# Performance work log

Hardware: AMD Instinct MI355X
Metric: run time of the kernel (lower is better)

The kernel has to match this reference:

```python
import jax, jax.numpy as jnp
import numpy as np

N, G, E, H, OUT, MAX_N = 131072, 256, 384, 6, 256, 1024
DH = E // H  # 64


def _make_sizes():
    # variable-length segments summing exactly to N, each in [1, MAX_N]
    rng = np.random.default_rng(0)
    raw = rng.integers(128, 896, G).astype(np.int64)
    diff = int(N - raw.sum())
    q, r = divmod(diff, G)
    sizes = raw + q
    sizes[:r] += 1
    assert sizes.sum() == N and sizes.min() >= 1 and sizes.max() <= MAX_N
    return sizes


def setup_inputs() -> dict:
    key = jax.random.key(0)
    ks = jax.random.split(key, 8)
    s = 1.0 / np.sqrt(E)
    return {
        "node_feat": jax.random.normal(ks[0], (N, E), jnp.float32),
        "sizes": jnp.asarray(_make_sizes(), jnp.int32),
        "query": jax.random.normal(ks[1], (E,), jnp.float32),
        "Wq": jax.random.normal(ks[2], (E, E), jnp.float32) * s,
        "bq": jnp.zeros((E,), jnp.float32),
        "Wk": jax.random.normal(ks[3], (E, E), jnp.float32) * s,
        "bk": jnp.zeros((E,), jnp.float32),
        "Wv": jax.random.normal(ks[4], (E, E), jnp.float32) * s,
        "bv": jnp.zeros((E,), jnp.float32),
        "Wo": jax.random.normal(ks[5], (E, E), jnp.float32) * s,
        "bo": jnp.zeros((E,), jnp.float32),
        "Wp": jax.random.normal(ks[6], (OUT, E), jnp.float32) * s,
        "bp": jnp.zeros((OUT,), jnp.float32),
    }


def reference(node_feat, sizes, query, Wq, bq, Wk, bk, Wv, bv, Wo, bo, Wp, bp):
    # segment offsets and padded gather indices
    offsets = jnp.cumsum(sizes) - sizes                      # [G]
    pos = jnp.arange(MAX_N)
    idx = jnp.clip(offsets[:, None] + pos[None, :], 0, N - 1)  # [G, MAX_N]
    mask = pos[None, :] < sizes[:, None]                     # [G, MAX_N]

    # project K/V on the flat node table (one big GEMM), then gather into padded form
    k_flat = node_feat @ Wk.T + bk                           # [N, E]
    v_flat = node_feat @ Wv.T + bv
    k = k_flat[idx].reshape(G, MAX_N, H, DH)
    v = v_flat[idx].reshape(G, MAX_N, H, DH)

    # single shared query token, pre-scaled (PyTorch MHA scales q by 1/sqrt(head_dim))
    q = ((query @ Wq.T + bq) * (1.0 / np.sqrt(DH))).reshape(H, DH)

    scores = jnp.einsum('hd,gnhd->ghn', q, k)                # [G, H, MAX_N]
    scores = jnp.where(mask[:, None, :], scores, -1e30)
    attn = jax.nn.softmax(scores, axis=-1)
    pooled = jnp.einsum('ghn,gnhd->ghd', attn, v).reshape(G, E)

    out = pooled @ Wo.T + bo                                 # MHA out_proj
    return out @ Wp.T + bp                                   # final proj  [G, OUT]
```

## Files before the change

### kernel.cpp

```cpp
#include <hip/hip_runtime.h>
#include <math.h>

#define NN 131072
#define G  256
#define E  384
#define H  6
#define DH 64
#define OUTD 256
#define MAXN 1024

#define SPLIT 4
#define PART_STRIDE 2316

#define WS_QK   0
#define WS_OFF  2432
#define WS_PART 12288
#define WS_WVT  (WS_PART + G*SPLIT*PART_STRIDE)
#define WS_WOT  (WS_WVT + E*E)
#define WS_WPT  (WS_WOT + E*E)

__global__ __launch_bounds__(256) void k_prep(
    const int* __restrict__ sizes, const float* __restrict__ query,
    const float* __restrict__ Wq, const float* __restrict__ bq,
    const float* __restrict__ Wk, const float* __restrict__ Wv,
    const float* __restrict__ Wo, const float* __restrict__ Wp,
    float* __restrict__ wsf) {
  const int b = blockIdx.x;
  const int tid = threadIdx.x;
  if (b == 0) {
    __shared__ int s_scan[G];
    const int sz = sizes[tid];
    s_scan[tid] = sz;
    __syncthreads();
    for (int d = 1; d < G; d <<= 1) {
      int t = (tid >= d) ? s_scan[tid - d] : 0;
      __syncthreads();
      s_scan[tid] += t;
      __syncthreads();
    }
    ((int*)(wsf + WS_OFF))[tid] = s_scan[tid] - sz;
  } else if (b <= 36) {
    const int h = (b - 1) / 6, ec = (b - 1) % 6;
    __shared__ float qv_s[64];
    __shared__ float qps[256];
    __shared__ float ps[256];
    {
      const int r = tid >> 2, q = tid & 3;
      const int row = h * 64 + r;
      float a = 0.f;
#pragma unroll 4
      for (int j = 0; j < 96; j++)
        a += Wq[(size_t)row * E + q * 96 + j] * query[q * 96 + j];
      qps[tid] = a;
    }
    __syncthreads();
    if (tid < 64)
      qv_s[tid] = 0.125f * (qps[tid * 4] + qps[tid * 4 + 1] +
                            qps[tid * 4 + 2] + qps[tid * 4 + 3] +
                            bq[h * 64 + tid]);
    __syncthreads();
    const int el = tid & 63, dq = tid >> 6;
    float a = 0.f;
#pragma unroll 4
    for (int d = dq * 16; d < dq * 16 + 16; d++)
      a += qv_s[d] * Wk[(size_t)(h * 64 + d) * E + ec * 64 + el];
    ps[tid] = a;
    __syncthreads();
    if (tid < 64)
      wsf[WS_QK + h * E + ec * 64 + tid] =
          ps[tid] + ps[64 + tid] + ps[128 + tid] + ps[192 + tid];
  } else {
    __shared__ float s[64][65];
    const int t = b - 37;
    const float* src;
    float* dst;
    int R, tr, tc;
    if (t < 36)      { src = Wv; dst = wsf + WS_WVT; R = 384; tr = t / 6;        tc = t % 6; }
    else if (t < 72) { src = Wo; dst = wsf + WS_WOT; R = 384; tr = (t - 36) / 6; tc = (t - 36) % 6; }
    else             { src = Wp; dst = wsf + WS_WPT; R = 256; tr = (t - 72) / 6; tc = (t - 72) % 6; }
    const int r0 = tr * 64, c0 = tc * 64;
#pragma unroll
    for (int k = 0; k < 16; k++) {
      int idx = k * 256 + tid;
      int r = idx >> 6, cc = idx & 63;
      s[r][cc] = src[(size_t)(r0 + r) * E + c0 + cc];
    }
    __syncthreads();
#pragma unroll
    for (int k = 0; k < 16; k++) {
      int idx = k * 256 + tid;
      int cc = idx >> 6, r = idx & 63;
      dst[(size_t)(c0 + cc) * R + r0 + r] = s[r][cc];
    }
  }
}

template <int CTRL>
__device__ __forceinline__ float dpp_radd(float v) {
  int t = __builtin_amdgcn_update_dpp(0, __float_as_int(v), CTRL, 0xf, 0xf, true);
  return v + __int_as_float(t);
}
__device__ __forceinline__ float wave_sum64(float v) {
  v = dpp_radd<0xB1>(v);
  v = dpp_radd<0x4E>(v);
  v = dpp_radd<0x141>(v);
  v = dpp_radd<0x140>(v);
  v += __shfl_xor(v, 16, 64);
  v += __shfl_xor(v, 32, 64);
  return v;
}

__global__ __launch_bounds__(768, 3) void k12s_quarter(
    const float* __restrict__ x, const int* __restrict__ sizes,
    float* __restrict__ wsf) {
  __shared__ float xsl[4][H * E];
  __shared__ float msh[12][H], lsh[12][H], wgts[12][H];
  __shared__ float Msh[H], Lsh[H];

  const int tid = threadIdx.x;
  const int lane = tid & 63;
  const int w = tid >> 6;
  const int b = blockIdx.x;
  const int g = b >> 2, q = b & 3;
  const int sz = sizes[g];
  const int qlen = (sz + 3) >> 2;
  const int start = q * qlen;
  int len = sz - start;
  if (len > qlen) len = qlen;
  if (len < 0) len = 0;
  const int n0 = ((const int*)(wsf + WS_OFF))[g] + start;

  float qk[6][6];
#pragma unroll
  for (int h = 0; h < 6; h++)
#pragma unroll
    for (int k = 0; k < 6; k++) qk[h][k] = wsf[WS_QK + h * E + k * 64 + lane];

  float m[6], l[6], acc[6][6];
#pragma unroll
  for (int h = 0; h < 6; h++) {
    m[h] = -3.0e38f;
    l[h] = 0.f;
#pragma unroll
    for (int k = 0; k < 6; k++) acc[h][k] = 0.f;
  }

  const float* xp = x + (size_t)(n0 + w) * E + lane;
  const int cnt = (len > w) ? ((len - w + 11) / 12) : 0;

  float x0[6], x1[6];
#define LOADX(buf, i)                                              \
  {                                                                \
    const float* p_ = xp + (size_t)(i) * (12 * E);                 \
    _Pragma("unroll") for (int k_ = 0; k_ < 6; k_++)               \
        buf[k_] = p_[k_ * 64];                                     \
  }
#define COMPUTE(xv)                                                          \
  {                                                                          \
    float sr[6];                                                             \
    _Pragma("unroll") for (int h_ = 0; h_ < 6; h_++) {                       \
      float a_ = qk[h_][0] * xv[0];                                          \
      _Pragma("unroll") for (int k_ = 1; k_ < 6; k_++)                       \
          a_ = fmaf(qk[h_][k_], xv[k_], a_);                                 \
      sr[h_] = a_;                                                           \
    }                                                                        \
    _Pragma("unroll") for (int h_ = 0; h_ < 6; h_++)                         \
        sr[h_] = wave_sum64(sr[h_]);                                         \
    bool upd_ = false;                                                       \
    _Pragma("unroll") for (int h_ = 0; h_ < 6; h_++)                         \
        upd_ = upd_ || (sr[h_] > m[h_] + 8.0f);                              \
    if (upd_) {                                                              \
      _Pragma("unroll") for (int h_ = 0; h_ < 6; h_++) {                     \
        const float nm_ = fmaxf(m[h_], sr[h_]);                              \
        const float f_ = __expf(m[h_] - nm_);                                \
        m[h_] = nm_;                                                         \
        l[h_] *= f_;                                                         \
        _Pragma("unroll") for (int k_ = 0; k_ < 6; k_++) acc[h_][k_] *= f_;  \
      }                                                                      \
    }                                                                        \
    _Pragma("unroll") for (int h_ = 0; h_ < 6; h_++) {                       \
      const float p_ = __expf(sr[h_] - m[h_]);                               \
      l[h_] += p_;                                                           \
      _Pragma("unroll") for (int k_ = 0; k_ < 6; k_++)                       \
          acc[h_][k_] = fmaf(p_, xv[k_], acc[h_][k_]);                       \
    }                                                                        \
  }

  if (cnt > 0) {
    LOADX(x0, 0);
    int i = 0;
    while (true) {
      int ip = (i + 1 < cnt) ? i + 1 : i;
      LOADX(x1, ip);
      COMPUTE(x0);
      if (++i >= cnt) break;
      ip = (i + 1 < cnt) ? i + 1 : i;
      LOADX(x0, ip);
      COMPUTE(x1);
      if (++i >= cnt) break;
    }
  }
#undef LOADX
#undef COMPUTE

  if (lane == 0) {
#pragma unroll
    for (int h = 0; h < 6; h++) {
      msh[w][h] = m[h];
      lsh[w][h] = l[h];
    }
  }
  __syncthreads();
  if (tid < 6) {
    const int h = tid;
    float M = -3.0e38f;
    for (int s = 0; s < 12; s++) M = fmaxf(M, msh[s][h]);
    float L = 0.f;
    for (int s = 0; s < 12; s++) {
      const float wv_ = __expf(msh[s][h] - M);
      wgts[s][h] = wv_;
      L += lsh[s][h] * wv_;
    }
    Msh[h] = M;
    Lsh[h] = L;
  }
  __syncthreads();
  {
    float wg[6];
#pragma unroll
    for (int h = 0; h < 6; h++) wg[h] = wgts[w][h];
#pragma unroll
    for (int h = 0; h < 6; h++)
#pragma unroll
      for (int k = 0; k < 6; k++) acc[h][k] *= wg[h];
  }
  {
    float* xs = &xsl[w & 3][0];
    if (w < 4) {
#pragma unroll
      for (int h = 0; h < 6; h++)
#pragma unroll
        for (int k = 0; k < 6; k++) xs[h * E + k * 64 + lane] = acc[h][k];
    }
    __syncthreads();
    if (w >= 4 && w < 8) {
#pragma unroll
      for (int h = 0; h < 6; h++)
#pragma unroll
        for (int k = 0; k < 6; k++) xs[h * E + k * 64 + lane] += acc[h][k];
    }
    __syncthreads();
    if (w >= 8) {
#pragma unroll
      for (int h = 0; h < 6; h++)
#pragma unroll
        for (int k = 0; k < 6; k++) xs[h * E + k * 64 + lane] += acc[h][k];
    }
    __syncthreads();
  }
  float* pslot = wsf + WS_PART + (size_t)b * PART_STRIDE;
  for (int idx = tid; idx < H * E; idx += 768) {
    pslot[idx] = (xsl[0][idx] + xsl[1][idx]) + (xsl[2][idx] + xsl[3][idx]);
  }
  if (tid < 6) {
    pslot[2304 + tid] = Msh[tid];
    pslot[2310 + tid] = Lsh[tid];
  }
}

__global__ __launch_bounds__(768) void k3c_group(
    const float* __restrict__ wsf,
    const float* __restrict__ bv, const float* __restrict__ bo,
    const float* __restrict__ bp, float* __restrict__ out) {
  __shared__ float xb[H * E];
  __shared__ float pooled[E];
  __shared__ float om[E];
  __shared__ float ps[768];
  __shared__ float msh[SPLIT][H], lsh[SPLIT][H], wgt[SPLIT][H];
  __shared__ float linv[H];
  const int tid = threadIdx.x;
  const int g = blockIdx.x;
  const float* pg = wsf + WS_PART + (size_t)(g * SPLIT) * PART_STRIDE;
  const float* wvt = wsf + WS_WVT;
  const float* wot = wsf + WS_WOT;
  const float* wpt = wsf + WS_WPT;

  if (tid < SPLIT * H) {
    const int s2 = tid / H, h2 = tid % H;
    msh[s2][h2] = pg[(size_t)s2 * PART_STRIDE + 2304 + h2];
    lsh[s2][h2] = pg[(size_t)s2 * PART_STRIDE + 2310 + h2];
  }
  __syncthreads();
  if (tid < H) {
    float M = -3.0e38f;
    for (int s = 0; s < SPLIT; s++) M = fmaxf(M, msh[s][tid]);
    float L = 0.f;
    for (int s = 0; s < SPLIT; s++) {
      const float wv_ = __expf(msh[s][tid] - M);
      wgt[s][tid] = wv_;
      L += lsh[s][tid] * wv_;
    }
    linv[tid] = 1.f / L;
  }
  __syncthreads();
  for (int idx = tid; idx < H * E; idx += 768) {
    const int h = idx / E;
    const float* pp = pg + idx;
    float a = pp[0] * wgt[0][h];
    a += pp[(size_t)1 * PART_STRIDE] * wgt[1][h];
    a += pp[(size_t)2 * PART_STRIDE] * wgt[2][h];
    a += pp[(size_t)3 * PART_STRIDE] * wgt[3][h];
    xb[idx] = a * linv[h];
  }
  __syncthreads();

  {
    const int i = tid % 384, ks = tid / 384;
    const float* xh = xb + (i >> 6) * E + ks * 192;
    const float* wp_ = wvt + (size_t)(ks * 192) * E + i;
    float a0 = 0.f, a1 = 0.f, a2 = 0.f, a3 = 0.f;
#pragma unroll 4
    for (int e = 0; e < 192; e += 4) {
      a0 += wp_[(size_t)(e + 0) * E] * xh[e + 0];
      a1 += wp_[(size_t)(e + 1) * E] * xh[e + 1];
      a2 += wp_[(size_t)(e + 2) * E] * xh[e + 2];
      a3 += wp_[(size_t)(e + 3) * E] * xh[e + 3];
    }
    ps[tid] = (a0 + a1) + (a2 + a3);
  }
  __syncthreads();
  if (tid < 384) pooled[tid] = ps[tid] + ps[384 + tid] + bv[tid];
  __syncthreads();

  {
    const int i = tid % 384, ks = tid / 384;
    const float* xh = pooled + ks * 192;
    const float* wp_ = wot + (size_t)(ks * 192) * E + i;
    float a0 = 0.f, a1 = 0.f, a2 = 0.f, a3 = 0.f;
#pragma unroll 4
    for (int e = 0; e < 192; e += 4) {
      a0 += wp_[(size_t)(e + 0) * E] * xh[e + 0];
      a1 += wp_[(size_t)(e + 1) * E] * xh[e + 1];
      a2 += wp_[(size_t)(e + 2) * E] * xh[e + 2];
      a3 += wp_[(size_t)(e + 3) * E] * xh[e + 3];
    }
    ps[tid] = (a0 + a1) + (a2 + a3);
  }
  __syncthreads();
  if (tid < 384) om[tid] = ps[tid] + ps[384 + tid] + bo[tid];
  __syncthreads();

  {
    const int o = tid % 256, ks = tid / 256;
    const float* xh = om + ks * 128;
    const float* wp_ = wpt + (size_t)(ks * 128) * OUTD + o;
    float a0 = 0.f, a1 = 0.f, a2 = 0.f, a3 = 0.f;
#pragma unroll 4
    for (int e = 0; e < 128; e += 4) {
      a0 += wp_[(size_t)(e + 0) * OUTD] * xh[e + 0];
      a1 += wp_[(size_t)(e + 1) * OUTD] * xh[e + 1];
      a2 += wp_[(size_t)(e + 2) * OUTD] * xh[e + 2];
      a3 += wp_[(size_t)(e + 3) * OUTD] * xh[e + 3];
    }
    ps[tid] = (a0 + a1) + (a2 + a3);
  }
  __syncthreads();
  if (tid < 256)
    out[(size_t)g * OUTD + tid] = ps[tid] + ps[256 + tid] + ps[512 + tid] + bp[tid];
}

extern "C" void kernel_launch(void* const* d_in, const int* in_sizes, int n_in,
                              void* d_out, int out_size, void* d_ws, size_t ws_size,
                              hipStream_t stream) {
  const float* x     = (const float*)d_in[0];
  const int*   sizes = (const int*)d_in[1];
  const float* query = (const float*)d_in[2];
  const float* Wq    = (const float*)d_in[3];
  const float* bq    = (const float*)d_in[4];
  const float* Wk    = (const float*)d_in[5];
  const float* bk    = (const float*)d_in[6];  (void)bk;
  const float* Wv    = (const float*)d_in[7];
  const float* bv    = (const float*)d_in[8];
  const float* Wo    = (const float*)d_in[9];
  const float* bo    = (const float*)d_in[10];
  const float* Wp    = (const float*)d_in[11];
  const float* bp    = (const float*)d_in[12];
  float* wsf = (float*)d_ws;
  float* out = (float*)d_out;

  hipLaunchKernelGGL(k_prep, dim3(133), dim3(256), 0, stream,
                     sizes, query, Wq, bq, Wk, Wv, Wo, Wp, wsf);
  hipLaunchKernelGGL(k12s_quarter, dim3(G * SPLIT), dim3(768), 0, stream,
                     x, sizes, wsf);
  hipLaunchKernelGGL(k3c_group, dim3(G), dim3(768), 0, stream,
                     wsf, bv, bo, bp, out);
}
```

Before: 337.2 us.

## Fuse group epilogue into split kernel via last-block atomic and split heads across waves

```diff
diff --git a/kernel.cpp b/kernel.cpp
--- a/kernel.cpp
+++ b/kernel.cpp
@@ -14,6 +14,7 @@
 
 #define WS_QK   0
 #define WS_OFF  2432
+#define WS_CNT  2688
 #define WS_PART 12288
 #define WS_WVT  (WS_PART + G*SPLIT*PART_STRIDE)
 #define WS_WOT  (WS_WVT + E*E)
@@ -31,6 +32,7 @@
     __shared__ int s_scan[G];
     const int sz = sizes[tid];
     s_scan[tid] = sz;
+    ((int*)(wsf + WS_CNT))[tid] = 0;
     __syncthreads();
     for (int d = 1; d < G; d <<= 1) {
       int t = (tid >= d) ? s_scan[tid - d] : 0;
@@ -110,16 +112,21 @@
   return v;
 }
 
-__global__ __launch_bounds__(768, 3) void k12s_quarter(
+__global__ __launch_bounds__(768, 4) void k12f_quarter(
     const float* __restrict__ x, const int* __restrict__ sizes,
+    const float* __restrict__ bv, const float* __restrict__ bo,
+    const float* __restrict__ bp, float* __restrict__ out,
     float* __restrict__ wsf) {
   __shared__ float xsl[4][H * E];
-  __shared__ float msh[12][H], lsh[12][H], wgts[12][H];
+  __shared__ float msh[12][3], lsh[12][3], wgts[12][3];
   __shared__ float Msh[H], Lsh[H];
+  __shared__ int s_last;
 
   const int tid = threadIdx.x;
   const int lane = tid & 63;
   const int w = tid >> 6;
+  const int sid = (w < 6) ? w : w - 6;
+  const int half = (w < 6) ? 0 : 1;
   const int b = blockIdx.x;
   const int g = b >> 2, q = b & 3;
   const int sz = sizes[g];
@@ -130,47 +137,48 @@
   if (len < 0) len = 0;
   const int n0 = ((const int*)(wsf + WS_OFF))[g] + start;
 
-  float qk[6][6];
-#pragma unroll
-  for (int h = 0; h < 6; h++)
-#pragma unroll
-    for (int k = 0; k < 6; k++) qk[h][k] = wsf[WS_QK + h * E + k * 64 + lane];
-
-  float m[6], l[6], acc[6][6];
-#pragma unroll
-  for (int h = 0; h < 6; h++) {
-    m[h] = -3.0e38f;
-    l[h] = 0.f;
-#pragma unroll
-    for (int k = 0; k < 6; k++) acc[h][k] = 0.f;
-  }
-
-  const float* xp = x + (size_t)(n0 + w) * E + lane;
-  const int cnt = (len > w) ? ((len - w + 11) / 12) : 0;
+  float qk[3][6];
+#pragma unroll
+  for (int hh = 0; hh < 3; hh++)
+#pragma unroll
+    for (int k = 0; k < 6; k++)
+      qk[hh][k] = wsf[WS_QK + (half * 3 + hh) * E + k * 64 + lane];
+
+  float m[3], l[3], acc[3][6];
+#pragma unroll
+  for (int hh = 0; hh < 3; hh++) {
+    m[hh] = -3.0e38f;
+    l[hh] = 0.f;
+#pragma unroll
+    for (int k = 0; k < 6; k++) acc[hh][k] = 0.f;
+  }
+
+  const float* xp = x + (size_t)(n0 + sid) * E + lane;
+  const int cnt = (len > sid) ? ((len - sid + 5) / 6) : 0;
 
   float x0[6], x1[6];
 #define LOADX(buf, i)                                              \
   {                                                                \
-    const float* p_ = xp + (size_t)(i) * (12 * E);                 \
+    const float* p_ = xp + (size_t)(i) * (6 * E);                  \
     _Pragma("unroll") for (int k_ = 0; k_ < 6; k_++)               \
         buf[k_] = p_[k_ * 64];                                     \
   }
 #define COMPUTE(xv)                                                          \
   {                                                                          \
-    float sr[6];                                                             \
-    _Pragma("unroll") for (int h_ = 0; h_ < 6; h_++) {                       \
+    float sr[3];                                                             \
+    _Pragma("unroll") for (int h_ = 0; h_ < 3; h_++) {                       \
       float a_ = qk[h_][0] * xv[0];                                          \
       _Pragma("unroll") for (int k_ = 1; k_ < 6; k_++)                       \
           a_ = fmaf(qk[h_][k_], xv[k_], a_);                                 \
       sr[h_] = a_;                                                           \
     }                                                                        \
-    _Pragma("unroll") for (int h_ = 0; h_ < 6; h_++)                         \
+    _Pragma("unroll") for (int h_ = 0; h_ < 3; h_++)                         \
         sr[h_] = wave_sum64(sr[h_]);                                         \
     bool upd_ = false;                                                       \
-    _Pragma("unroll") for (int h_ = 0; h_ < 6; h_++)                         \
+    _Pragma("unroll") for (int h_ = 0; h_ < 3; h_++)                         \
         upd_ = upd_ || (sr[h_] > m[h_] + 8.0f);                              \
     if (upd_) {                                                              \
-      _Pragma("unroll") for (int h_ = 0; h_ < 6; h_++) {                     \
+      _Pragma("unroll") for (int h_ = 0; h_ < 3; h_++) {                     \
         const float nm_ = fmaxf(m[h_], sr[h_]);                              \
         const float f_ = __expf(m[h_] - nm_);                                \
         m[h_] = nm_;                                                         \
@@ -178,7 +186,7 @@
         _Pragma("unroll") for (int k_ = 0; k_ < 6; k_++) acc[h_][k_] *= f_;  \
       }                                                                      \
     }                                                                        \
-    _Pragma("unroll") for (int h_ = 0; h_ < 6; h_++) {                       \
+    _Pragma("unroll") for (int h_ = 0; h_ < 3; h_++) {                       \
       const float p_ = __expf(sr[h_] - m[h_]);                               \
       l[h_] += p_;                                                           \
       _Pragma("unroll") for (int k_ = 0; k_ < 6; k_++)                       \
@@ -205,56 +213,54 @@
 
   if (lane == 0) {
 #pragma unroll
-    for (int h = 0; h < 6; h++) {
-      msh[w][h] = m[h];
-      lsh[w][h] = l[h];
+    for (int hh = 0; hh < 3; hh++) {
+      msh[w][hh] = m[hh];
+      lsh[w][hh] = l[hh];
     }
   }
   __syncthreads();
   if (tid < 6) {
-    const int h = tid;
+    const int h = tid, hf = h / 3, hh = h % 3;
     float M = -3.0e38f;
-    for (int s = 0; s < 12; s++) M = fmaxf(M, msh[s][h]);
+    for (int s = 0; s < 6; s++) M = fmaxf(M, msh[hf * 6 + s][hh]);
     float L = 0.f;
-    for (int s = 0; s < 12; s++) {
-      const float wv_ = __expf(msh[s][h] - M);
-      wgts[s][h] = wv_;
-      L += lsh[s][h] * wv_;
+    for (int s = 0; s < 6; s++) {
+      const float wv_ = __expf(msh[hf * 6 + s][hh] - M);
+      wgts[hf * 6 + s][hh] = wv_;
+      L += lsh[hf * 6 + s][hh] * wv_;
     }
     Msh[h] = M;
     Lsh[h] = L;
   }
   __syncthreads();
   {
-    float wg[6];
-#pragma unroll
-    for (int h = 0; h < 6; h++) wg[h] = wgts[w][h];
-#pragma unroll
-    for (int h = 0; h < 6; h++)
-#pragma unroll
-      for (int k = 0; k < 6; k++) acc[h][k] *= wg[h];
+    float wg[3];
+#pragma unroll
+    for (int hh = 0; hh < 3; hh++) wg[hh] = wgts[w][hh];
+#pragma unroll
+    for (int hh = 0; hh < 3; hh++)
+#pragma unroll
+      for (int k = 0; k < 6; k++) acc[hh][k] *= wg[hh];
   }
   {
-    float* xs = &xsl[w & 3][0];
-    if (w < 4) {
-#pragma unroll
-      for (int h = 0; h < 6; h++)
-#pragma unroll
-        for (int k = 0; k < 6; k++) xs[h * E + k * 64 + lane] = acc[h][k];
-    }
-    __syncthreads();
-    if (w >= 4 && w < 8) {
-#pragma unroll
-      for (int h = 0; h < 6; h++)
-#pragma unroll
-        for (int k = 0; k < 6; k++) xs[h * E + k * 64 + lane] += acc[h][k];
-    }
-    __syncthreads();
-    if (w >= 8) {
-#pragma unroll
-      for (int h = 0; h < 6; h++)
-#pragma unroll
-        for (int k = 0; k < 6; k++) xs[h * E + k * 64 + lane] += acc[h][k];
+    const int slot = sid;
+    const int hbase = half * 3;
+    if (slot < 4) {
+      float* xs = &xsl[slot][0];
+#pragma unroll
+      for (int hh = 0; hh < 3; hh++)
+#pragma unroll
+        for (int k = 0; k < 6; k++)
+          xs[(hbase + hh) * E + k * 64 + lane] = acc[hh][k];
+    }
+    __syncthreads();
+    if (slot >= 4) {
+      float* xs = &xsl[slot - 4][0];
+#pragma unroll
+      for (int hh = 0; hh < 3; hh++)
+#pragma unroll
+        for (int k = 0; k < 6; k++)
+          xs[(hbase + hh) * E + k * 64 + lane] += acc[hh][k];
     }
     __syncthreads();
   }
@@ -266,20 +272,23 @@
     pslot[2304 + tid] = Msh[tid];
     pslot[2310 + tid] = Lsh[tid];
   }
-}
-
-__global__ __launch_bounds__(768) void k3c_group(
-    const float* __restrict__ wsf,
-    const float* __restrict__ bv, const float* __restrict__ bo,
-    const float* __restrict__ bp, float* __restrict__ out) {
-  __shared__ float xb[H * E];
-  __shared__ float pooled[E];
-  __shared__ float om[E];
-  __shared__ float ps[768];
-  __shared__ float msh[SPLIT][H], lsh[SPLIT][H], wgt[SPLIT][H];
+
+  __threadfence();
+  __syncthreads();
+  if (tid == 0) {
+    const int old = atomicAdd(&((int*)(wsf + WS_CNT))[g], 1);
+    s_last = (old == SPLIT - 1) ? 1 : 0;
+  }
+  __syncthreads();
+  if (!s_last) return;
+  __threadfence();
+
+  __shared__ float msh2[SPLIT][H], lsh2[SPLIT][H], wgt2[SPLIT][H];
   __shared__ float linv[H];
-  const int tid = threadIdx.x;
-  const int g = blockIdx.x;
+  float* xb = &xsl[0][0];
+  float* pooled = &xsl[1][0];
+  float* om = &xsl[1][0] + 384;
+  float* ps = &xsl[1][0] + 768;
   const float* pg = wsf + WS_PART + (size_t)(g * SPLIT) * PART_STRIDE;
   const float* wvt = wsf + WS_WVT;
   const float* wot = wsf + WS_WOT;
@@ -287,18 +296,18 @@
 
   if (tid < SPLIT * H) {
     const int s2 = tid / H, h2 = tid % H;
-    msh[s2][h2] = pg[(size_t)s2 * PART_STRIDE + 2304 + h2];
-    lsh[s2][h2] = pg[(size_t)s2 * PART_STRIDE + 2310 + h2];
+    msh2[s2][h2] = pg[(size_t)s2 * PART_STRIDE + 2304 + h2];
+    lsh2[s2][h2] = pg[(size_t)s2 * PART_STRIDE + 2310 + h2];
   }
   __syncthreads();
   if (tid < H) {
     float M = -3.0e38f;
-    for (int s = 0; s < SPLIT; s++) M = fmaxf(M, msh[s][tid]);
+    for (int s = 0; s < SPLIT; s++) M = fmaxf(M, msh2[s][tid]);
     float L = 0.f;
     for (int s = 0; s < SPLIT; s++) {
-      const float wv_ = __expf(msh[s][tid] - M);
-      wgt[s][tid] = wv_;
-      L += lsh[s][tid] * wv_;
+      const float wv_ = __expf(msh2[s][tid] - M);
+      wgt2[s][tid] = wv_;
+      L += lsh2[s][tid] * wv_;
     }
     linv[tid] = 1.f / L;
   }
@@ -306,10 +315,10 @@
   for (int idx = tid; idx < H * E; idx += 768) {
     const int h = idx / E;
     const float* pp = pg + idx;
-    float a = pp[0] * wgt[0][h];
-    a += pp[(size_t)1 * PART_STRIDE] * wgt[1][h];
-    a += pp[(size_t)2 * PART_STRIDE] * wgt[2][h];
-    a += pp[(size_t)3 * PART_STRIDE] * wgt[3][h];
+    float a = pp[0] * wgt2[0][h];
+    a += pp[(size_t)1 * PART_STRIDE] * wgt2[1][h];
+    a += pp[(size_t)2 * PART_STRIDE] * wgt2[2][h];
+    a += pp[(size_t)3 * PART_STRIDE] * wgt2[3][h];
     xb[idx] = a * linv[h];
   }
   __syncthreads();
@@ -390,8 +399,6 @@
 
   hipLaunchKernelGGL(k_prep, dim3(133), dim3(256), 0, stream,
                      sizes, query, Wq, bq, Wk, Wv, Wo, Wp, wsf);
-  hipLaunchKernelGGL(k12s_quarter, dim3(G * SPLIT), dim3(768), 0, stream,
-                     x, sizes, wsf);
-  hipLaunchKernelGGL(k3c_group, dim3(G), dim3(768), 0, stream,
-                     wsf, bv, bo, bp, out);
+  hipLaunchKernelGGL(k12f_quarter, dim3(G * SPLIT), dim3(768), 0, stream,
+                     x, sizes, bv, bo, bp, out, wsf);
 }
```

Measured after the change: 1.029 ms. 3.05x slower.
